# Kernel tuning notes

Hardware: AMD Instinct MI355X
Metric: run time of the kernel (lower is better)

The kernel has to match this reference:

```python
import jax, jax.numpy as jnp
import numpy as np

B, H, Wd, CIN = 4, 64, 64, 65   # batch, height, width, in_channels (incl. time)
COUT = 256                      # out_channels (incl. time)
K = 3
KK = K * K
PAD, STRIDE = 1, 1
SOUT = 4                        # output_stabilizer_size (C4 rotations)
CURV = 1.0                      # Lorentz manifold curvature k
LIN_FEAT = (CIN - 1) * KK + 1   # 577


def make_c4_z2_indices(ksize):
    # (out_rotation, in_stabilizer=1, u, v, [s, u_src, v_src]) index table,
    # realizing the C4 filter rotation as a gather (as in GrouPy).
    f = np.arange(ksize * ksize).reshape(ksize, ksize)
    inds = np.zeros((4, 1, ksize, ksize, 3), dtype=np.int64)
    for r in range(4):
        rot = np.rot90(f, r)
        u, v = np.unravel_index(rot, (ksize, ksize))
        inds[r, 0, :, :, 1] = u
        inds[r, 0, :, :, 2] = v
    return inds

INDS = make_c4_z2_indices(K)


def setup_inputs() -> dict:
    key = jax.random.key(0)
    k1, k2, k3 = jax.random.split(key, 3)
    stdv = float(np.sqrt(2.0 / ((CIN - 1) * KK)))  # reset_parameters
    x = jax.random.normal(k1, (B, H, Wd, CIN), dtype=jnp.float32)
    W = jax.random.uniform(k2, (COUT, LIN_FEAT), minval=-stdv, maxval=stdv, dtype=jnp.float32)
    b = jax.random.uniform(k3, (COUT,), minval=-stdv, maxval=stdv, dtype=jnp.float32)
    return {"x": x, "W": W, "b": b}


def _unfold(x):
    # x: (B, C, H, W) -> (B, C*KK, Ho*Wo) in torch.nn.Unfold layout (channel-major, kernel-minor)
    xp = jnp.pad(x, ((0, 0), (0, 0), (PAD, PAD), (PAD, PAD)))
    ho = (H + 2 * PAD - K) // STRIDE + 1
    wo = (Wd + 2 * PAD - K) // STRIDE + 1
    cols = [xp[:, :, i:i + ho * STRIDE:STRIDE, j:j + wo * STRIDE:STRIDE]
            for i in range(K) for j in range(K)]
    p = jnp.stack(cols, axis=2)  # (B, C, KK, ho, wo)
    return p.reshape(B, CIN * KK, ho * wo), ho, wo


def _forward(x, W, b):
    # torch code does x.view(B, C, H, W) on channel-last data: a reshape, not a permute.
    xv = x.reshape(B, CIN, H, Wd)
    patches, ho, wo = _unfold(xv)
    patches = jnp.transpose(patches, (0, 2, 1))          # (B, P, C*KK)
    P = patches.shape[1]
    patches = patches.reshape(B, P, CIN, 1, K, K)
    patches = jnp.broadcast_to(patches, (B, P, CIN, SOUT, K, K))  # repeat over group dim
    # --- group-equivariant filter transform realized as a gather on patches ---
    ir = INDS.reshape(-1, 3)                              # (SOUT*KK, 3)
    pi = patches[:, :, :, ir[:, 0], ir[:, 1], ir[:, 2]]   # (B, P, C, SOUT*KK)
    pi = pi.reshape(B, P, CIN, SOUT, KK)
    pt = jnp.transpose(pi, (3, 0, 1, 2, 4)).reshape(SOUT, B, P, CIN * KK)
    # --- extract_lorentz_patches (vectorized over group dim) ---
    sqrt_k = jnp.sqrt(jnp.float32(CURV))
    t = jnp.maximum(pt[..., :KK], sqrt_k)                 # clamp time components
    t_resc = jnp.sqrt(jnp.sum(t * t, axis=-1, keepdims=True) - (KK - 1) * CURV)
    sp = pt[..., KK:]                                     # (SOUT,B,P,(C-1)*KK) channel-major
    sp = sp.reshape(SOUT, B, P, CIN - 1, KK).swapaxes(-1, -2).reshape(SOUT, B, P, (CIN - 1) * KK)
    pre = jnp.concatenate([t_resc, sp], axis=-1)          # (SOUT,B,P,LIN_FEAT)
    # --- LorentzFullyConnected: linear, then recompute time from space norm ---
    y = jnp.einsum('gbpf,of->gbpo', pre, W) + b           # (SOUT,B,P,COUT)
    y_sp = y[..., 1:]
    y_t = jnp.sqrt(jnp.sum(y_sp * y_sp, axis=-1, keepdims=True) + CURV)
    out = jnp.concatenate([y_t, y_sp], axis=-1)
    out = jnp.transpose(out, (1, 0, 2, 3)).reshape(B, SOUT, ho, wo, COUT)
    return out


def reference(x, W, b):
    return _forward(x, W, b)
```

## Files before the change

### kernel.cpp

```cpp
#include <hip/hip_runtime.h>
#include <hip/hip_bf16.h>

#define CIN 65
#define LIN 577
#define NSTEP 18
#define M_  16384

typedef __bf16 bf16x8 __attribute__((ext_vector_type(8)));
typedef float  f32x4  __attribute__((ext_vector_type(4)));
typedef unsigned short u16x8 __attribute__((ext_vector_type(8)));

__constant__ int SIG[4][9] = {
  {0,1,2,3,4,5,6,7,8},
  {2,5,8,1,4,7,0,3,6},
  {8,7,6,5,4,3,2,1,0},
  {6,3,0,7,4,1,8,5,2}};

__device__ __forceinline__ int swzm(int r) { return (r ^ (r >> 2)) & 3; }

__global__ __launch_bounds__(512) void prep_k(const float* __restrict__ x,
                                              const float* __restrict__ W,
                                              __hip_bfloat16* __restrict__ A,
                                              __hip_bfloat16* __restrict__ Wg,
                                              float* __restrict__ T) {
  __shared__ float lds[CIN * 3 * 72];
  const int tid = threadIdx.x;
  if (blockIdx.x >= 256) {
    int pidx = (blockIdx.x - 256) * 512 + tid;
    int jc  = pidx & 3;
    int col = (pidx >> 2) & 255;
    int t   = pidx >> 10;
    int ks  = t % NSTEP, g = t / NSTEP;
    int k   = SIG[(4 - g) & 3][ks >> 1];
    const float* src = W + col * LIN + 1 + k * 64 + (ks & 1) * 32 + jc * 8;
    u16x8 pk;
#pragma unroll
    for (int e = 0; e < 8; ++e) {
      union { __hip_bfloat16 h; unsigned short u; } cv;
      cv.h = __float2bfloat16(src[e]);
      pk[e] = cv.u;
    }
    *(u16x8*)(Wg + (size_t)pidx * 8) = pk;
    return;
  }
  const int b = blockIdx.x >> 6, py = blockIdx.x & 63;
  const float* xb = x + (size_t)b * (CIN * 4096);
  for (int i = tid; i < CIN * 3 * 18; i += 512)
    *(f32x4*)&lds[i * 4] = (f32x4){0.f, 0.f, 0.f, 0.f};
  __syncthreads();
  for (int i = tid; i < CIN * 3 * 16; i += 512) {
    int pr = i >> 4, j = i & 15;
    int c = pr / 3, dy = pr - c * 3;
    int hy = py + dy - 1;
    if (hy >= 0 && hy < 64)
      *(f32x4*)&lds[c * 216 + dy * 72 + 4 + j * 4] =
          *(const f32x4*)(xb + c * 4096 + hy * 64 + j * 4);
  }
  __syncthreads();

  const int wave = tid >> 6, px = tid & 63;
  const int rowid = (blockIdx.x << 6) | px;
#pragma unroll
  for (int qi = 0; qi < 9; ++qi) {
    int q = wave * 9 + qi;
    int m = q >> 3, cb8 = q & 7;
    int dy = m / 3, dx = m - dy * 3;
    const float* src = &lds[(1 + cb8 * 8) * 216 + dy * 72 + 3 + dx + px];
    u16x8 pk;
#pragma unroll
    for (int e = 0; e < 8; ++e) {
      union { __hip_bfloat16 h; unsigned short u; } cv;
      cv.h = __float2bfloat16(src[e * 216]);
      pk[e] = cv.u;
    }
    *(u16x8*)(A + ((size_t)q * M_ + rowid) * 8) = pk;
  }
  if (wave == 0) {
    float s = 0.f;
#pragma unroll
    for (int m = 0; m < 9; ++m) {
      float t = fmaxf(lds[(m / 3) * 72 + 3 + (m % 3) + px], 1.f);
      s += t * t;
    }
    T[rowid] = sqrtf(s - 8.f);
  }
}

__device__ __forceinline__ void async_cp16(const void* g, void* ldsbase) {
  __builtin_amdgcn_global_load_lds(
      (const __attribute__((address_space(1))) void*)g,
      (__attribute__((address_space(3))) void*)ldsbase, 16, 0, 0);
}

__global__ __launch_bounds__(512, 4) void gemm_k(const __hip_bfloat16* __restrict__ A,
                                                 const __hip_bfloat16* __restrict__ Wg,
                                                 const float* __restrict__ W,
                                                 const float* __restrict__ bias,
                                                 const float* __restrict__ T,
                                                 float* __restrict__ out) {
  __shared__ __align__(16) char smem[73728];
  const int fid = blockIdx.x;
  const int lid = ((fid & 7) << 6) | (fid >> 3);
  const int g = lid & 3, rb = lid >> 2;
  const int brow = rb << 7;
  const int tid = threadIdx.x, wave = tid >> 6, lane = tid & 63;
  const int fr = lane & 15, fq = lane >> 4;
  const int wr = (wave >> 2) * 64, wcb = (wave & 3) * 64;

  const int arow = tid >> 2;
  const int alc  = (tid & 3) ^ swzm(arow);
  const int bcol0 = tid >> 2;
  const int blc0  = (tid & 3) ^ swzm(bcol0);
  const int bcol1 = 128 + (tid >> 2);
  const int blc1  = (tid & 3) ^ swzm(bcol1);
  f32x4 acc[4][4] = {};

  auto STAGE = [&](char* pa, char* pb, int ks) {
    int qb = (ks >> 1) * 8 + (ks & 1) * 4;
    async_cp16(A + (((size_t)(qb + alc) * M_ + brow + arow) << 3), pa + wave * 1024);
    const __hip_bfloat16* bs = Wg + ((size_t)(g * NSTEP + ks) << 13);
    async_cp16(bs + bcol0 * 32 + blc0 * 8, pb + wave * 1024);
    async_cp16(bs + bcol1 * 32 + blc1 * 8, pb + wave * 1024 + 8192);
  };
  auto COMPUTE = [&](const char* Ab, const char* Bb) {
    bf16x8 af[4], bf[4];
#pragma unroll
    for (int i = 0; i < 4; ++i) {
      int r = wr + i * 16 + fr;
      af[i] = *(const bf16x8*)(Ab + r * 64 + ((fq ^ swzm(r)) << 4));
    }
#pragma unroll
    for (int j = 0; j < 4; ++j) {
      int c = wcb + j * 16 + fr;
      bf[j] = *(const bf16x8*)(Bb + c * 64 + ((fq ^ swzm(c)) << 4));
    }
    __builtin_amdgcn_s_setprio(1);
#pragma unroll
    for (int i = 0; i < 4; ++i)
#pragma unroll
      for (int j = 0; j < 4; ++j)
        acc[i][j] = __builtin_amdgcn_mfma_f32_16x16x32_bf16(af[i], bf[j], acc[i][j], 0, 0, 0);
    __builtin_amdgcn_s_setprio(0);
  };

  float* Tsh = (float*)smem;
  char *cA = smem,         *nA = smem + 8192,  *tA = smem + 16384;
  char *cB = smem + 24576, *nB = smem + 40960, *tB = smem + 57344;
  STAGE(cA, cB, 0);
  STAGE(nA, nB, 1);
  for (int ks = 0; ks < NSTEP; ++ks) {
    if (ks < NSTEP - 1) {
      asm volatile("s_waitcnt vmcnt(3)" ::: "memory");
    } else {
      asm volatile("s_waitcnt vmcnt(0)" ::: "memory");
    }
    __builtin_amdgcn_s_barrier();
    if (ks + 2 < NSTEP) STAGE(tA, tB, ks + 2);
    if (ks == NSTEP - 1 && tid < 128) Tsh[tid] = T[brow + tid];
    COMPUTE(cA, cB);
    char* r = cA; cA = nA; nA = tA; tA = r;
    r = cB; cB = nB; nB = tB; tB = r;
  }
  __syncthreads();

  float* Ps = (float*)(smem + 512);
  float bo[4], w0v[4]; int oc[4];
#pragma unroll
  for (int j = 0; j < 4; ++j) {
    oc[j]  = wcb + j * 16 + fr;
    bo[j]  = bias[oc[j]];
    w0v[j] = W[oc[j] * LIN];
  }
#pragma unroll
  for (int i = 0; i < 4; ++i) {
#pragma unroll
    for (int rr = 0; rr < 4; ++rr) {
      int rl = wr + i * 16 + fq * 4 + rr;
      int row = brow + rl;
      size_t obase = ((size_t)(((row >> 12) * 4 + g) * 4096 + (row & 4095)) << 8);
      float tval = Tsh[rl];
      float s = 0.f;
#pragma unroll
      for (int j = 0; j < 4; ++j) {
        float y = acc[i][j][rr] + bo[j] + tval * w0v[j];
        if (oc[j] != 0) { s += y * y; out[obase + oc[j]] = y; }
      }
      s += __shfl_xor(s, 1); s += __shfl_xor(s, 2);
      s += __shfl_xor(s, 4); s += __shfl_xor(s, 8);
      if (fr == 0) Ps[rl * 4 + (wave & 3)] = s;
    }
  }
  __syncthreads();
  if (tid < 128) {
    int row = brow + tid;
    float s = Ps[tid * 4] + Ps[tid * 4 + 1] + Ps[tid * 4 + 2] + Ps[tid * 4 + 3] + 1.0f;
    out[(size_t)(((row >> 12) * 4 + g) * 4096 + (row & 4095)) << 8] = sqrtf(s);
  }
}

extern "C" void kernel_launch(void* const* d_in, const int* in_sizes, int n_in,
                              void* d_out, int out_size, void* d_ws, size_t ws_size,
                              hipStream_t stream) {
  const float* x    = (const float*)d_in[0];
  const float* W    = (const float*)d_in[1];
  const float* bias = (const float*)d_in[2];
  float* out = (float*)d_out;

  char* ws = (char*)d_ws;
  __hip_bfloat16* Wg = (__hip_bfloat16*)ws;
  float*          T  = (float*)(ws + 1179648);
  __hip_bfloat16* A  = (__hip_bfloat16*)(ws + 1245184);

  prep_k<<<400, 512, 0, stream>>>(x, W, A, Wg, T);
  gemm_k<<<512, 512, 0, stream>>>(A, Wg, W, bias, T, out);
}
```

Before: 43.48 us.

## Load A fragments directly into registers and keep only B in LDS

The GEMM kernel stops staging the A (patch) operand through LDS. Each wave now loads its A MFMA fragments straight from global memory into registers, double-buffered across two register sets. The B (weight) operand stays triple-buffered in LDS with async copies, and the loop is unrolled by two with adjusted vmcnt waits. This removes the LDS write and read traffic for A and shrinks the LDS footprint, which may let more blocks fit per CU. The cost is that each A tile is now fetched from global or cache by four waves instead of once, and the kernel relies on the compiler's wait counting for the register loads.

After: 43.86 us. No clear change (+0.9%).

```diff
diff --git a/kernel.cpp b/kernel.cpp
--- a/kernel.cpp
+++ b/kernel.cpp
@@ -98,7 +98,7 @@
                                                  const float* __restrict__ bias,
                                                  const float* __restrict__ T,
                                                  float* __restrict__ out) {
-  __shared__ __align__(16) char smem[73728];
+  __shared__ __align__(16) char smem[51712];
   const int fid = blockIdx.x;
   const int lid = ((fid & 7) << 6) | (fid >> 3);
   const int g = lid & 3, rb = lid >> 2;
@@ -107,28 +107,29 @@
   const int fr = lane & 15, fq = lane >> 4;
   const int wr = (wave >> 2) * 64, wcb = (wave & 3) * 64;
 
-  const int arow = tid >> 2;
-  const int alc  = (tid & 3) ^ swzm(arow);
-  const int bcol0 = tid >> 2;
-  const int blc0  = (tid & 3) ^ swzm(bcol0);
-  const int bcol1 = 128 + (tid >> 2);
-  const int blc1  = (tid & 3) ^ swzm(bcol1);
-  f32x4 acc[4][4] = {};
-
-  auto STAGE = [&](char* pa, char* pb, int ks) {
-    int qb = (ks >> 1) * 8 + (ks & 1) * 4;
-    async_cp16(A + (((size_t)(qb + alc) * M_ + brow + arow) << 3), pa + wave * 1024);
-    const __hip_bfloat16* bs = Wg + ((size_t)(g * NSTEP + ks) << 13);
+  float* Tsh = (float*)(smem + 49152);
+  float* Ps  = (float*)(smem + 49664);
+  if (tid < 128) Tsh[tid] = T[brow + tid];
+
+  const int bcol0 = tid >> 2, blc0 = (tid & 3) ^ swzm(bcol0);
+  const int bcol1 = 128 + (tid >> 2), blc1 = (tid & 3) ^ swzm(bcol1);
+  const __hip_bfloat16* Wgg = Wg + ((size_t)(g * NSTEP) << 13);
+  auto STAGE_B = [&](char* pb, int ks) {
+    const __hip_bfloat16* bs = Wgg + ((size_t)ks << 13);
     async_cp16(bs + bcol0 * 32 + blc0 * 8, pb + wave * 1024);
     async_cp16(bs + bcol1 * 32 + blc1 * 8, pb + wave * 1024 + 8192);
   };
-  auto COMPUTE = [&](const char* Ab, const char* Bb) {
-    bf16x8 af[4], bf[4];
-#pragma unroll
-    for (int i = 0; i < 4; ++i) {
-      int r = wr + i * 16 + fr;
-      af[i] = *(const bf16x8*)(Ab + r * 64 + ((fq ^ swzm(r)) << 4));
-    }
+
+  const __hip_bfloat16* Arow = A + (((size_t)fq * M_ + brow + wr + fr) << 3);
+  auto LOAD_A = [&](bf16x8* dst, int ks) {
+#pragma unroll
+    for (int i = 0; i < 4; ++i)
+      dst[i] = *(const bf16x8*)(Arow + (size_t)ks * (M_ * 32) + i * 128);
+  };
+
+  f32x4 acc[4][4] = {};
+  auto COMPUTE = [&](const char* Bb, const bf16x8* af) {
+    bf16x8 bf[4];
 #pragma unroll
     for (int j = 0; j < 4; ++j) {
       int c = wcb + j * 16 + fr;
@@ -143,27 +144,32 @@
     __builtin_amdgcn_s_setprio(0);
   };
 
-  float* Tsh = (float*)smem;
-  char *cA = smem,         *nA = smem + 8192,  *tA = smem + 16384;
-  char *cB = smem + 24576, *nB = smem + 40960, *tB = smem + 57344;
-  STAGE(cA, cB, 0);
-  STAGE(nA, nB, 1);
-  for (int ks = 0; ks < NSTEP; ++ks) {
-    if (ks < NSTEP - 1) {
-      asm volatile("s_waitcnt vmcnt(3)" ::: "memory");
+  bf16x8 afA[4], afB[4];
+  char *cB = smem, *nB = smem + 16384, *tB = smem + 32768;
+  STAGE_B(cB, 0);
+  STAGE_B(nB, 1);
+  LOAD_A(afA, 0);
+
+  for (int kp = 0; kp < NSTEP; kp += 2) {
+    asm volatile("s_waitcnt vmcnt(6)" ::: "memory");
+    __builtin_amdgcn_s_barrier();
+    if (kp + 2 < NSTEP) STAGE_B(tB, kp + 2);
+    LOAD_A(afB, kp + 1);
+    COMPUTE(cB, afA);
+    { char* r = cB; cB = nB; nB = tB; tB = r; }
+    if (kp + 1 < NSTEP - 1) {
+      asm volatile("s_waitcnt vmcnt(6)" ::: "memory");
     } else {
-      asm volatile("s_waitcnt vmcnt(0)" ::: "memory");
+      asm volatile("s_waitcnt vmcnt(4)" ::: "memory");
     }
     __builtin_amdgcn_s_barrier();
-    if (ks + 2 < NSTEP) STAGE(tA, tB, ks + 2);
-    if (ks == NSTEP - 1 && tid < 128) Tsh[tid] = T[brow + tid];
-    COMPUTE(cA, cB);
-    char* r = cA; cA = nA; nA = tA; tA = r;
-    r = cB; cB = nB; nB = tB; tB = r;
-  }
-  __syncthreads();
-
-  float* Ps = (float*)(smem + 512);
+    if (kp + 3 < NSTEP) STAGE_B(tB, kp + 3);
+    if (kp + 2 < NSTEP) LOAD_A(afA, kp + 2);
+    COMPUTE(cB, afB);
+    { char* r = cB; cB = nB; nB = tB; tB = r; }
+  }
+  __syncthreads();
+
   float bo[4], w0v[4]; int oc[4];
 #pragma unroll
   for (int j = 0; j < 4; ++j) {
```

## Enlarge GEMM tile to 256x256 with K=64 steps and phased double-buffering

Applied to the files above, without the earlier changes.

Each GEMM block now computes a 256-row by 256-column tile with a K depth of 64 per step (9 steps instead of 18), and the weight-prep layout is changed to match. The main loop is split into four phases that interleave LDS fragment loads, async global-to-LDS prefetch of the next tile and MFMA bursts under explicit barriers, with double buffering. The intent is more operand reuse per load and fewer barrier and loop iterations. In exchange it uses 128KB of LDS and more accumulator registers, so occupancy drops and only 256 blocks are launched, about one per CU.

Measured after the change: 48.17 us. 1.11x slower.

```diff
diff --git a/kernel.cpp b/kernel.cpp
--- a/kernel.cpp
+++ b/kernel.cpp
@@ -3,7 +3,7 @@
 
 #define CIN 65
 #define LIN 577
-#define NSTEP 18
+#define NT  9
 #define M_  16384
 
 typedef __bf16 bf16x8 __attribute__((ext_vector_type(8)));
@@ -15,8 +15,6 @@
   {2,5,8,1,4,7,0,3,6},
   {8,7,6,5,4,3,2,1,0},
   {6,3,0,7,4,1,8,5,2}};
-
-__device__ __forceinline__ int swzm(int r) { return (r ^ (r >> 2)) & 3; }
 
 __global__ __launch_bounds__(512) void prep_k(const float* __restrict__ x,
                                               const float* __restrict__ W,
@@ -27,12 +25,12 @@
   const int tid = threadIdx.x;
   if (blockIdx.x >= 256) {
     int pidx = (blockIdx.x - 256) * 512 + tid;
-    int jc  = pidx & 3;
-    int col = (pidx >> 2) & 255;
-    int t   = pidx >> 10;
-    int ks  = t % NSTEP, g = t / NSTEP;
-    int k   = SIG[(4 - g) & 3][ks >> 1];
-    const float* src = W + col * LIN + 1 + k * 64 + (ks & 1) * 32 + jc * 8;
+    int jc  = pidx & 7;
+    int col = (pidx >> 3) & 255;
+    int t   = pidx >> 11;
+    int m   = t % NT, g = t / NT;
+    int k   = SIG[(4 - g) & 3][m];
+    const float* src = W + col * LIN + 1 + k * 64 + jc * 8;
     u16x8 pk;
 #pragma unroll
     for (int e = 0; e < 8; ++e) {
@@ -92,78 +90,114 @@
       (__attribute__((address_space(3))) void*)ldsbase, 16, 0, 0);
 }
 
-__global__ __launch_bounds__(512, 4) void gemm_k(const __hip_bfloat16* __restrict__ A,
+__global__ __launch_bounds__(512, 2) void gemm_k(const __hip_bfloat16* __restrict__ A,
                                                  const __hip_bfloat16* __restrict__ Wg,
                                                  const float* __restrict__ W,
                                                  const float* __restrict__ bias,
                                                  const float* __restrict__ T,
                                                  float* __restrict__ out) {
-  __shared__ __align__(16) char smem[73728];
+  __shared__ __align__(16) char smem[131072];
   const int fid = blockIdx.x;
-  const int lid = ((fid & 7) << 6) | (fid >> 3);
+  const int lid = ((fid & 7) << 5) | (fid >> 3);
   const int g = lid & 3, rb = lid >> 2;
-  const int brow = rb << 7;
+  const int brow = rb << 8;
   const int tid = threadIdx.x, wave = tid >> 6, lane = tid & 63;
   const int fr = lane & 15, fq = lane >> 4;
-  const int wr = (wave >> 2) * 64, wcb = (wave & 3) * 64;
-
-  const int arow = tid >> 2;
-  const int alc  = (tid & 3) ^ swzm(arow);
-  const int bcol0 = tid >> 2;
-  const int blc0  = (tid & 3) ^ swzm(bcol0);
-  const int bcol1 = 128 + (tid >> 2);
-  const int blc1  = (tid & 3) ^ swzm(bcol1);
-  f32x4 acc[4][4] = {};
-
-  auto STAGE = [&](char* pa, char* pb, int ks) {
-    int qb = (ks >> 1) * 8 + (ks & 1) * 4;
-    async_cp16(A + (((size_t)(qb + alc) * M_ + brow + arow) << 3), pa + wave * 1024);
-    const __hip_bfloat16* bs = Wg + ((size_t)(g * NSTEP + ks) << 13);
-    async_cp16(bs + bcol0 * 32 + blc0 * 8, pb + wave * 1024);
-    async_cp16(bs + bcol1 * 32 + blc1 * 8, pb + wave * 1024 + 8192);
-  };
-  auto COMPUTE = [&](const char* Ab, const char* Bb) {
-    bf16x8 af[4], bf[4];
+  const int wr = (wave >> 2) * 128, wcb = (wave & 3) * 64;
+  const __hip_bfloat16* Wgb = Wg + ((size_t)(g * NT) << 14);
+  f32x4 acc[8][4] = {};
+
+  auto STAGE_A = [&](char* slot, int kt, int l0) {
+#pragma unroll
+    for (int l = l0; l < l0 + 2; ++l) {
+      int u = l * 512 + tid, r = u >> 3, lc = (u & 7) ^ (r & 7);
+      async_cp16(A + (((size_t)(kt * 8 + lc) * M_ + brow + r) << 3),
+                 slot + (l * 512 + wave * 64) * 16);
+    }
+  };
+  auto STAGE_B = [&](char* slot, int kt, int l0) {
+#pragma unroll
+    for (int l = l0; l < l0 + 2; ++l) {
+      int u = l * 512 + tid, c = u >> 3, lc = (u & 7) ^ (c & 7);
+      async_cp16(Wgb + ((size_t)kt << 14) + c * 64 + lc * 8,
+                 slot + (l * 512 + wave * 64) * 16);
+    }
+  };
+  auto LDA = [&](const char* As, bf16x8* af, int kk, int ih) {
 #pragma unroll
     for (int i = 0; i < 4; ++i) {
-      int r = wr + i * 16 + fr;
-      af[i] = *(const bf16x8*)(Ab + r * 64 + ((fq ^ swzm(r)) << 4));
-    }
+      int r = wr + ih * 64 + i * 16 + fr;
+      af[i] = *(const bf16x8*)(As + r * 128 + (((kk * 4 + fq) ^ (r & 7)) << 4));
+    }
+  };
+  auto LDB = [&](const char* Bs, bf16x8* bf, int kk) {
 #pragma unroll
     for (int j = 0; j < 4; ++j) {
       int c = wcb + j * 16 + fr;
-      bf[j] = *(const bf16x8*)(Bb + c * 64 + ((fq ^ swzm(c)) << 4));
-    }
+      bf[j] = *(const bf16x8*)(Bs + c * 128 + (((kk * 4 + fq) ^ (c & 7)) << 4));
+    }
+  };
+  auto MM = [&](const bf16x8* af, const bf16x8* bf, int ih) {
     __builtin_amdgcn_s_setprio(1);
 #pragma unroll
     for (int i = 0; i < 4; ++i)
 #pragma unroll
       for (int j = 0; j < 4; ++j)
-        acc[i][j] = __builtin_amdgcn_mfma_f32_16x16x32_bf16(af[i], bf[j], acc[i][j], 0, 0, 0);
+        acc[ih * 4 + i][j] =
+            __builtin_amdgcn_mfma_f32_16x16x32_bf16(af[i], bf[j], acc[ih * 4 + i][j], 0, 0, 0);
     __builtin_amdgcn_s_setprio(0);
   };
 
-  float* Tsh = (float*)smem;
-  char *cA = smem,         *nA = smem + 8192,  *tA = smem + 16384;
-  char *cB = smem + 24576, *nB = smem + 40960, *tB = smem + 57344;
-  STAGE(cA, cB, 0);
-  STAGE(nA, nB, 1);
-  for (int ks = 0; ks < NSTEP; ++ks) {
-    if (ks < NSTEP - 1) {
-      asm volatile("s_waitcnt vmcnt(3)" ::: "memory");
-    } else {
-      asm volatile("s_waitcnt vmcnt(0)" ::: "memory");
-    }
-    __builtin_amdgcn_s_barrier();
-    if (ks + 2 < NSTEP) STAGE(tA, tB, ks + 2);
-    if (ks == NSTEP - 1 && tid < 128) Tsh[tid] = T[brow + tid];
-    COMPUTE(cA, cB);
-    char* r = cA; cA = nA; nA = tA; tA = r;
-    r = cB; cB = nB; nB = tB; tB = r;
-  }
-  __syncthreads();
-
-  float* Ps = (float*)(smem + 512);
+  STAGE_A(smem, 0, 0); STAGE_A(smem, 0, 2);
+  STAGE_B(smem + 65536, 0, 0); STAGE_B(smem + 65536, 0, 2);
+  asm volatile("s_waitcnt vmcnt(0)" ::: "memory");
+  __builtin_amdgcn_s_barrier();
+  __builtin_amdgcn_sched_barrier(0);
+
+  for (int kt = 0; kt < NT; ++kt) {
+    const int cb = (kt & 1) * 32768, nb = 32768 - cb;
+    const char* As = smem + cb;
+    const char* Bs = smem + 65536 + cb;
+    char* An = smem + nb;
+    char* Bn = smem + 65536 + nb;
+    const bool pf = (kt + 1 < NT);
+    bf16x8 af[4], bf[4];
+    LDA(As, af, 0, 0); LDB(Bs, bf, 0);
+    if (pf) STAGE_A(An, kt + 1, 0);
+    __builtin_amdgcn_s_barrier();
+    asm volatile("s_waitcnt lgkmcnt(0)" ::: "memory");
+    __builtin_amdgcn_sched_barrier(0);
+    MM(af, bf, 0);
+    __builtin_amdgcn_s_barrier();
+    __builtin_amdgcn_sched_barrier(0);
+    LDA(As, af, 0, 1);
+    if (pf) STAGE_A(An, kt + 1, 2);
+    __builtin_amdgcn_s_barrier();
+    asm volatile("s_waitcnt lgkmcnt(0)" ::: "memory");
+    __builtin_amdgcn_sched_barrier(0);
+    MM(af, bf, 1);
+    __builtin_amdgcn_s_barrier();
+    __builtin_amdgcn_sched_barrier(0);
+    LDA(As, af, 1, 0); LDB(Bs, bf, 1);
+    if (pf) STAGE_B(Bn, kt + 1, 0);
+    __builtin_amdgcn_s_barrier();
+    asm volatile("s_waitcnt lgkmcnt(0)" ::: "memory");
+    __builtin_amdgcn_sched_barrier(0);
+    MM(af, bf, 0);
+    __builtin_amdgcn_s_barrier();
+    __builtin_amdgcn_sched_barrier(0);
+    LDA(As, af, 1, 1);
+    if (pf) STAGE_B(Bn, kt + 1, 2);
+    __builtin_amdgcn_s_barrier();
+    asm volatile("s_waitcnt lgkmcnt(0)" ::: "memory");
+    __builtin_amdgcn_sched_barrier(0);
+    MM(af, bf, 1);
+    asm volatile("s_waitcnt vmcnt(0)" ::: "memory");
+    __builtin_amdgcn_s_barrier();
+    __builtin_amdgcn_sched_barrier(0);
+  }
+
+  float* Ps = (float*)smem;
   float bo[4], w0v[4]; int oc[4];
 #pragma unroll
   for (int j = 0; j < 4; ++j) {
@@ -172,13 +206,13 @@
     w0v[j] = W[oc[j] * LIN];
   }
 #pragma unroll
-  for (int i = 0; i < 4; ++i) {
+  for (int i = 0; i < 8; ++i) {
 #pragma unroll
     for (int rr = 0; rr < 4; ++rr) {
       int rl = wr + i * 16 + fq * 4 + rr;
       int row = brow + rl;
       size_t obase = ((size_t)(((row >> 12) * 4 + g) * 4096 + (row & 4095)) << 8);
-      float tval = Tsh[rl];
+      float tval = T[row];
       float s = 0.f;
 #pragma unroll
       for (int j = 0; j < 4; ++j) {
@@ -191,7 +225,7 @@
     }
   }
   __syncthreads();
-  if (tid < 128) {
+  if (tid < 256) {
     int row = brow + tid;
     float s = Ps[tid * 4] + Ps[tid * 4 + 1] + Ps[tid * 4 + 2] + Ps[tid * 4 + 3] + 1.0f;
     out[(size_t)(((row >> 12) * 4 + g) * 4096 + (row & 4095)) << 8] = sqrtf(s);
@@ -212,5 +246,5 @@
   __hip_bfloat16* A  = (__hip_bfloat16*)(ws + 1245184);
 
   prep_k<<<400, 512, 0, stream>>>(x, W, A, Wg, T);
-  gemm_k<<<512, 512, 0, stream>>>(A, Wg, W, bias, T, out);
-}
+  gemm_k<<<256, 512, 0, stream>>>(A, Wg, W, bias, T, out);
+}
```
